# Kernel optimization log

Measured on AMD Instinct MI355X. Metric: run time of the kernel, lower is better.

The kernel has to match this reference:

```python
import jax, jax.numpy as jnp
import numpy as np

B, N, E, D, NS, H = 32, 4096, 256, 256, 8, 256
N_ITERS, N_SH, N_MESH, MESH_LR = 3, 5, 4, 5.0

def layer_norm(x, scale, bias, eps=1e-5):
    m = jnp.mean(x, axis=-1, keepdims=True)
    v = jnp.var(x, axis=-1, keepdims=True)
    return (x - m) / jnp.sqrt(v + eps) * scale + bias

def sinkhorn(C, a, b, u=None, v=None, n_iters=N_SH):
    # log-domain Sinkhorn with marginals a [B,N], b [B,S]; C [B,N,S]
    log_a, log_b = jnp.log(a), jnp.log(b)
    if u is None:
        u = jnp.zeros_like(a)
    if v is None:
        v = jnp.zeros_like(b)
    K = -C
    for _ in range(n_iters):
        u = log_a - jax.nn.logsumexp(K + v[:, None, :], axis=-1)
        v = log_b - jax.nn.logsumexp(K + u[:, :, None], axis=-2)
    attn = jnp.exp(K + u[:, :, None] + v[:, None, :])
    return attn, u, v

def minimize_entropy_of_sinkhorn(C0, a, b, mesh_lr=MESH_LR, n_mesh=N_MESH):
    # MESH: gradient-descend the cost matrix to minimize entropy of the transport plan
    def ent(C):
        attn, _, _ = sinkhorn(C, a, b)
        return -jnp.sum(attn * jnp.log(attn + 1e-8))
    C = C0
    for _ in range(n_mesh):
        C = C - mesh_lr * jax.grad(ent)(C)
    _, u, v = sinkhorn(C, a, b)
    return C, u, v

def gru_cell(x, h, Wih, Whh, bih, bhh):
    # torch.nn.GRUCell math, gate order (r, z, n)
    gi = x @ Wih.T + bih
    gh = h @ Whh.T + bhh
    ir, iz, inn = jnp.split(gi, 3, axis=-1)
    hr, hz, hn = jnp.split(gh, 3, axis=-1)
    r = jax.nn.sigmoid(ir + hr)
    z = jax.nn.sigmoid(iz + hz)
    n = jnp.tanh(inn + r * hn)
    return (1.0 - z) * n + z * h

def setup_inputs():
    key = jax.random.key(0)
    ks = jax.random.split(key, 16)
    s = 0.02
    return {
        "inputs": jax.random.normal(ks[0], (B, N, E), jnp.float32),
        "slots_init": jax.random.normal(ks[1], (B, NS, D), jnp.float32),
        "ln_in_s": jnp.ones((E,), jnp.float32), "ln_in_b": jnp.zeros((E,), jnp.float32),
        "ln_sl_s": jnp.ones((D,), jnp.float32), "ln_sl_b": jnp.zeros((D,), jnp.float32),
        "ln_mlp_s": jnp.ones((D,), jnp.float32), "ln_mlp_b": jnp.zeros((D,), jnp.float32),
        "Wq": jax.random.normal(ks[2], (D, D), jnp.float32) * s,
        "Wk": jax.random.normal(ks[3], (E, D), jnp.float32) * s,
        "Wv": jax.random.normal(ks[4], (E, D), jnp.float32) * s,
        "wi_W": jax.random.normal(ks[5], (E, 1), jnp.float32) * s, "wi_b": jnp.zeros((1,), jnp.float32),
        "ws_W": jax.random.normal(ks[6], (D, 1), jnp.float32) * s, "ws_b": jnp.zeros((1,), jnp.float32),
        "gru_Wih": jax.random.normal(ks[7], (3 * D, D), jnp.float32) * s,
        "gru_Whh": jax.random.normal(ks[8], (3 * D, D), jnp.float32) * s,
        "gru_bih": jnp.zeros((3 * D,), jnp.float32), "gru_bhh": jnp.zeros((3 * D,), jnp.float32),
        "mlp_W1": jax.random.normal(ks[9], (D, H), jnp.float32) * s, "mlp_b1": jnp.zeros((H,), jnp.float32),
        "mlp_W2": jax.random.normal(ks[10], (H, D), jnp.float32) * s, "mlp_b2": jnp.zeros((D,), jnp.float32),
    }

def reference(inputs, slots_init, ln_in_s, ln_in_b, ln_sl_s, ln_sl_b, ln_mlp_s, ln_mlp_b, Wq, Wk, Wv, wi_W, wi_b, ws_W, ws_b, gru_Wih, gru_Whh, gru_bih, gru_bhh, mlp_W1, mlp_b1, mlp_W2, mlp_b2):
    x = layer_norm(inputs, ln_in_s, ln_in_b)
    k = x @ Wk          # [B,N,D]
    v = x @ Wv          # [B,N,D]
    a = jax.nn.softmax(jnp.squeeze(x @ wi_W, -1) + wi_b[0], axis=-1) * NS  # input marginal [B,N]
    k_sq = jnp.sum(k * k, axis=-1)  # [B,N]

    def step(slots):
        sn = layer_norm(slots, ln_sl_s, ln_sl_b)
        b = jax.nn.softmax(jnp.squeeze(sn @ ws_W, -1) + ws_b[0], axis=-1) * NS  # slot marginal [B,S]
        q = sn @ Wq  # [B,S,D]
        # Euclidean cdist(k, q) via the Gram-matrix identity
        d2 = k_sq[:, :, None] + jnp.sum(q * q, -1)[:, None, :] - 2.0 * jnp.einsum('bnd,bsd->bns', k, q)
        C = jnp.sqrt(jnp.clip(d2, 1e-12))
        C, p, qpot = minimize_entropy_of_sinkhorn(C, a, b)
        attn, _, _ = sinkhorn(C, a, b, u=p, v=qpot)  # warm-started final sinkhorn
        updates = jnp.einsum('bns,bnd->bsd', attn, v)
        h = gru_cell(updates.reshape(-1, D), slots.reshape(-1, D), gru_Wih, gru_Whh, gru_bih, gru_bhh).reshape(B, NS, D)
        hn = layer_norm(h, ln_mlp_s, ln_mlp_b)
        h = h + (jax.nn.relu(hn @ mlp_W1 + mlp_b1) @ mlp_W2 + mlp_b2)
        return h, attn

    slots = slots_init
    attn = None
    for _ in range(N_ITERS - 1):
        slots, attn = step(slots)
    slots = jax.lax.stop_gradient(slots)  # .detach() before final step
    slots, attn = step(slots)
    return slots, jnp.transpose(attn, (0, 2, 1)), slots
```

## Files before the change

kernel.cpp:

```cpp
#include <hip/hip_runtime.h>
#include <hip/hip_bf16.h>

#define B_ 32
#define N_ 4096
#define E_ 256
#define D_ 256
#define NS_ 8
#define LN8 2.0794415416798357f
#define OFF_ATTN 65536
#define OFF_S2   (65536 + 1048576)
#define NSPLIT 8
#define SENT 0xFFFFFFFFu

typedef unsigned short u16;
typedef unsigned short u16x8 __attribute__((ext_vector_type(8)));
typedef __bf16 bf16x8 __attribute__((ext_vector_type(8)));
typedef float floatx4 __attribute__((ext_vector_type(4)));

__device__ __forceinline__ float bf2f(u16 h) {
  unsigned int u = ((unsigned int)h) << 16;
  return __uint_as_float(u);
}
__device__ __forceinline__ u16 f2bf(float f) {
  unsigned int u = __float_as_uint(f);
  unsigned int r = (u + 0x7FFFu + ((u >> 16) & 1u)) >> 16;
  return (u16)r;
}
__device__ __forceinline__ float ldx(const void* p, int i, int dt) {
  return dt ? ((const float*)p)[i] : bf2f(((const u16*)p)[i]);
}
__device__ __forceinline__ void stx(void* p, size_t i, int dt, float v) {
  if (dt) ((float*)p)[i] = v; else ((u16*)p)[i] = f2bf(v);
}
__device__ __forceinline__ float slog(float x) { return __logf(fmaxf(x, 1e-35f)); }
__device__ __forceinline__ float cl(float x) { return fminf(fmaxf(x, -1e30f), 1e30f); }

__device__ __forceinline__ float breduce256(float v, float* red4, int tid) {
  #pragma unroll
  for (int m = 1; m < 64; m <<= 1) v += __shfl_xor(v, m, 64);
  __syncthreads();
  if ((tid & 63) == 0) red4[tid >> 6] = v;
  __syncthreads();
  return red4[0] + red4[1] + red4[2] + red4[3];
}

__device__ __forceinline__ float breduce768(float v, float* red4, int tid) {
  #pragma unroll
  for (int m = 1; m < 64; m <<= 1) v += __shfl_xor(v, m, 64);
  __syncthreads();
  if (tid < 256 && (tid & 63) == 0) red4[tid >> 6] = v;
  __syncthreads();
  return red4[0] + red4[1] + red4[2] + red4[3];
}

__global__ void detect_dtype_kernel(const u16* __restrict__ inp, int* __restrict__ flag) {
  int lane = threadIdx.x & 63;
  int good = 0;
  for (int i = lane; i < 256; i += 64) {
    float x = bf2f(inp[i]);
    float ax = fabsf(x);
    if (x == 0.0f || (ax >= 1e-3f && ax <= 64.0f)) good++;
  }
  #pragma unroll
  for (int m = 1; m < 64; m <<= 1) good += __shfl_xor(good, m, 64);
  if (lane == 0) *flag = (good >= 208) ? 0 : 1;
}


__global__ void tr_kv_kernel(const void* __restrict__ Wk, const void* __restrict__ Wv,
                             u16* __restrict__ WkvT, const int* __restrict__ dtf) {
  const int dt = *dtf;
  int idx = blockIdx.x * 256 + threadIdx.x;
  int half = idx >> 16, i = idx & 65535;
  int r = i >> 8, c = i & 255;
  const void* src = half ? Wv : Wk;
  WkvT[((size_t)(half * 256 + c)) * 256 + r] = f2bf(ldx(src, i, dt));
}

__global__ void cast_w_kernel(const void* __restrict__ Wih, const void* __restrict__ Whh,
                              u16* __restrict__ WihB, u16* __restrict__ WhhB,
                              const int* __restrict__ dtf) {
  const int dt = *dtf;
  int idx = blockIdx.x * 256 + threadIdx.x;
  int half = idx >= 196608;
  int i = idx - (half ? 196608 : 0);
  u16* dst = half ? WhhB : WihB;
  dst[i] = f2bf(ldx(half ? Whh : Wih, i, dt));
}

__global__ void cast_slots_kernel(const void* __restrict__ src, float* __restrict__ dst,
                                  const int* __restrict__ dtf) {
  const int dt = *dtf;
  int i = blockIdx.x * 256 + threadIdx.x;
  dst[i] = ldx(src, i, dt);
}

__global__ __launch_bounds__(256) void ln_stats_kernel(
    const void* __restrict__ inp, const void* __restrict__ lns, const void* __restrict__ lnb,
    const void* __restrict__ wiW, const int* __restrict__ dtf,
    u16* __restrict__ xln, float* __restrict__ logits) {
  const int dt = *dtf;
  int row = blockIdx.x * 4 + (threadIdx.x >> 6);
  int lane = threadIdx.x & 63;
  float xs[4];
  if (dt) {
    float4 h = *(const float4*)((const float*)inp + (size_t)row * E_ + lane * 4);
    xs[0] = h.x; xs[1] = h.y; xs[2] = h.z; xs[3] = h.w;
  } else {
    ushort4 h = *(const ushort4*)((const u16*)inp + (size_t)row * E_ + lane * 4);
    xs[0] = bf2f(h.x); xs[1] = bf2f(h.y); xs[2] = bf2f(h.z); xs[3] = bf2f(h.w);
  }
  float s = xs[0] + xs[1] + xs[2] + xs[3];
  float q = xs[0]*xs[0] + xs[1]*xs[1] + xs[2]*xs[2] + xs[3]*xs[3];
  #pragma unroll
  for (int m = 1; m < 64; m <<= 1) { s += __shfl_xor(s, m, 64); q += __shfl_xor(q, m, 64); }
  float mean = s * (1.0f / E_);
  float var = q * (1.0f / E_) - mean * mean;
  float rstd = rsqrtf(fmaxf(var, 0.0f) + 1e-5f);
  int e = lane * 4;
  float d = 0.0f;
  float xn[4];
  #pragma unroll
  for (int j = 0; j < 4; ++j) {
    xn[j] = (xs[j] - mean) * rstd * ldx(lns, e + j, dt) + ldx(lnb, e + j, dt);
    d += xn[j] * ldx(wiW, e + j, dt);
  }
  ushort4 o;
  o.x = f2bf(xn[0]); o.y = f2bf(xn[1]); o.z = f2bf(xn[2]); o.w = f2bf(xn[3]);
  *(ushort4*)(xln + (size_t)row * E_ + e) = o;
  #pragma unroll
  for (int m = 1; m < 64; m <<= 1) d += __shfl_xor(d, m, 64);
  if (lane == 0) logits[row] = d;
}

__global__ __launch_bounds__(1024) void amarg_kernel(const float* __restrict__ logits,
    float* __restrict__ log_a, float* __restrict__ inva) {
  __shared__ float red[16];
  __shared__ float bcast;
  int b = blockIdx.x, tid = threadIdx.x;
  logits += (size_t)b * N_;
  float l[4];
  #pragma unroll
  for (int i = 0; i < 4; ++i) l[i] = logits[tid + i * 1024];
  float mx = fmaxf(fmaxf(l[0], l[1]), fmaxf(l[2], l[3]));
  #pragma unroll
  for (int m = 1; m < 64; m <<= 1) mx = fmaxf(mx, __shfl_xor(mx, m, 64));
  __syncthreads();
  if ((tid & 63) == 0) red[tid >> 6] = mx;
  __syncthreads();
  if (tid == 0) { float v = red[0]; for (int i = 1; i < 16; ++i) v = fmaxf(v, red[i]); bcast = v; }
  __syncthreads();
  float M = bcast;
  float se = 0.0f;
  #pragma unroll
  for (int i = 0; i < 4; ++i) se += __expf(l[i] - M);
  #pragma unroll
  for (int m = 1; m < 64; m <<= 1) se += __shfl_xor(se, m, 64);
  __syncthreads();
  if ((tid & 63) == 0) red[tid >> 6] = se;
  __syncthreads();
  if (tid == 0) { float v = 0; for (int i = 0; i < 16; ++i) v += red[i]; bcast = v; }
  __syncthreads();
  float lgS = slog(bcast);
  #pragma unroll
  for (int i = 0; i < 4; ++i) {
    float lav = l[i] - M - lgS + LN8;
    log_a[tid + i * 1024] = lav;
    inva[tid + i * 1024] = fminf(__expf(-lav), 1e20f);
  }
}

__global__ __launch_bounds__(256, 2) void gemm_bt_kernel(
    const u16* __restrict__ A, const u16* __restrict__ BT,
    u16* __restrict__ kbf, u16* __restrict__ vbf) {
  __shared__ __align__(16) u16 Als[128 * 32];
  __shared__ __align__(16) u16 Bls[128 * 32];
  int tid = threadIdx.x;
  int m0 = blockIdx.x * 128, n0 = blockIdx.y * 128;
  u16* ob = (n0 < 256) ? kbf : vbf;
  int nb = n0 & 255;
  int w = tid >> 6, lane = tid & 63;
  int wm = (w & 1) * 64, wn = (w >> 1) * 64;
  int fr = lane & 15, kg = lane >> 4;
  floatx4 acc[4][4];
  #pragma unroll
  for (int i = 0; i < 4; ++i)
    #pragma unroll
    for (int j = 0; j < 4; ++j) acc[i][j] = (floatx4){0.f, 0.f, 0.f, 0.f};
  int sm = tid >> 1;
  int sk0 = (tid & 1) * 16;
  const u16* arow = A + (size_t)(m0 + sm) * E_;
  const u16* brow = BT + (size_t)(n0 + sm) * E_;
  for (int kc = 0; kc < E_; kc += 32) {
    #pragma unroll
    for (int j = 0; j < 16; j += 8) {
      int kk = kc + sk0 + j;
      *(u16x8*)&Als[sm * 32 + sk0 + j] = *(const u16x8*)(arow + kk);
      *(u16x8*)&Bls[sm * 32 + sk0 + j] = *(const u16x8*)(brow + kk);
    }
    __syncthreads();
    bf16x8 af[4], bfv[4];
    #pragma unroll
    for (int im = 0; im < 4; ++im) af[im] = *(const bf16x8*)&Als[(wm + im * 16 + fr) * 32 + kg * 8];
    #pragma unroll
    for (int in = 0; in < 4; ++in) bfv[in] = *(const bf16x8*)&Bls[(wn + in * 16 + fr) * 32 + kg * 8];
    #pragma unroll
    for (int im = 0; im < 4; ++im)
      #pragma unroll
      for (int in = 0; in < 4; ++in)
        acc[im][in] = __builtin_amdgcn_mfma_f32_16x16x32_bf16(af[im], bfv[in], acc[im][in], 0, 0, 0);
    __syncthreads();
  }
  #pragma unroll
  for (int im = 0; im < 4; ++im)
    #pragma unroll
    for (int in = 0; in < 4; ++in)
      #pragma unroll
      for (int r = 0; r < 4; ++r) {
        int row = m0 + wm + im * 16 + kg * 4 + r;
        int col = nb + wn + in * 16 + fr;
        ob[(size_t)row * D_ + col] = f2bf(acc[im][in][r]);
      }
}


__global__ __launch_bounds__(256) void s1_kernel(
    const float* __restrict__ slots, const void* __restrict__ lnss, const void* __restrict__ lnsb,
    const void* __restrict__ Wq, const void* __restrict__ wsW, const int* __restrict__ dtf,
    float* __restrict__ qf, float* __restrict__ q_sq, float* __restrict__ logits_b) {
  __shared__ float sn_sh[256];
  __shared__ float red4[4];
  const int dt = *dtf;
  int row = blockIdx.x;
  int tid = threadIdx.x;
  float h = slots[(size_t)row * D_ + tid];
  float sum = breduce256(h, red4, tid);
  float sq = breduce256(h * h, red4, tid);
  float mean = sum * (1.0f / D_), var = sq * (1.0f / D_) - mean * mean;
  float rstd = rsqrtf(fmaxf(var, 0.0f) + 1e-5f);
  float sn = (h - mean) * rstd * ldx(lnss, tid, dt) + ldx(lnsb, tid, dt);
  sn_sh[tid] = sn;
  __syncthreads();
  float acc = 0.0f;
  if (dt) {
    const float* W = (const float*)Wq;
    for (int d = 0; d < 256; ++d) acc += sn_sh[d] * W[d * 256 + tid];
  } else {
    const u16* W = (const u16*)Wq;
    for (int d = 0; d < 256; ++d) acc += sn_sh[d] * bf2f(W[d * 256 + tid]);
  }
  qf[(size_t)row * 256 + tid] = acc;
  float qs = breduce256(acc * acc, red4, tid);
  float lbp = breduce256(sn * ldx(wsW, tid, dt), red4, tid);
  if (tid == 0) { q_sq[row] = qs; logits_b[row] = lbp; }
}

__device__ __forceinline__ float grp_sync_reduce(
    float acc8[8], float (*red)[8],
    unsigned int* gp, int rp, int blkn, int wv, int lane, int tid) {
  #pragma unroll
  for (int m = 1; m < 64; m <<= 1)
    #pragma unroll
    for (int s = 0; s < 8; ++s) acc8[s] += __shfl_xor(acc8[s], m, 64);
  if (lane == 0)
    #pragma unroll
    for (int s = 0; s < 8; ++s) red[wv][s] = acc8[s];
  __syncthreads();
  float x = 0.0f;
  if (tid < 64) {
    float v = red[tid >> 3][tid & 7];
    v += __shfl_xor(v, 8, 64);
    v += __shfl_xor(v, 16, 64);
    v += __shfl_xor(v, 32, 64);
    if (tid < 8)
      __hip_atomic_store(gp + rp * 64 + blkn * 8 + tid, __float_as_uint(v),
                         __ATOMIC_RELAXED, __HIP_MEMORY_SCOPE_AGENT);
    unsigned int u;
    for (;;) {
      u = __hip_atomic_load(gp + rp * 64 + tid, __ATOMIC_RELAXED, __HIP_MEMORY_SCOPE_AGENT);
      if (__all(u != SENT)) break;
      __builtin_amdgcn_s_sleep(1);
    }
    x = __uint_as_float(u);
    x += __shfl_xor(x, 8, 64);
    x += __shfl_xor(x, 16, 64);
    x += __shfl_xor(x, 32, 64);
  }
  return x;
}

__global__ __launch_bounds__(512, 2) void mesh_kernel(
    const u16* __restrict__ kbf, const u16* __restrict__ vbf,
    const float* __restrict__ qf32, const float* __restrict__ qsq_g,
    const float* __restrict__ log_a_g, const float* __restrict__ inva_g,
    const float* __restrict__ logits_b_g, const void* __restrict__ wsb,
    const int* __restrict__ dtf,
    unsigned int* __restrict__ gpart,
    float* __restrict__ updp, void* __restrict__ dout_or_null) {
  const int blkn = blockIdx.x;
  const int b = blockIdx.y;
  const int tid = threadIdx.x;
  const int dt = *dtf;
  const int n = blkn * 512 + tid;

  __shared__ float evP[6][8];
  __shared__ float lb[8], invb[8];
  __shared__ float dv[8];
  __shared__ float red[8][8];
  __shared__ float q_lds[8][256];
  __shared__ float qsq_l[8];
  __shared__ float pv_lds[512][8];

  const float la = log_a_g[(size_t)b * N_ + n];
  const float ia = inva_g[(size_t)b * N_ + n];
  unsigned int* gp = gpart + (size_t)b * 64 * 64;

  {
    const float* qb = qf32 + (size_t)b * 8 * 256;
    #pragma unroll
    for (int i = tid; i < 2048; i += 512) q_lds[i >> 8][i & 255] = qb[i];
    if (tid < 8) {
      qsq_l[tid] = qsq_g[b * 8 + tid];
      float off = ldx(wsb, 0, dt);
      float l[8], M = -1e30f;
      #pragma unroll
      for (int s = 0; s < 8; ++s) { l[s] = logits_b_g[b * 8 + s] + off; M = fmaxf(M, l[s]); }
      float S = 0.0f;
      #pragma unroll
      for (int s = 0; s < 8; ++s) S += __expf(l[s] - M);
      float lgS = slog(S);
      float x = l[tid] - M - lgS + LN8;
      lb[tid] = x; invb[tid] = fminf(__expf(-x), 1e20f);
    }
  }
  __syncthreads();

  float E[8], dK[8], eus[5];
  float eu = 0.0f, dup = 0.0f;
  {
    const u16* kp = kbf + ((size_t)b * N_ + n) * D_;
    float accq[8] = {0, 0, 0, 0, 0, 0, 0, 0};
    float kq = 0.0f;
    for (int kc = 0; kc < 256; kc += 8) {
      u16x8 kv = *(const u16x8*)(kp + kc);
      float kf[8];
      #pragma unroll
      for (int j = 0; j < 8; ++j) { kf[j] = bf2f(kv[j]); kq += kf[j] * kf[j]; }
      #pragma unroll
      for (int s = 0; s < 8; ++s) {
        float4 qa = *(const float4*)&q_lds[s][kc];
        float4 qb2 = *(const float4*)&q_lds[s][kc + 4];
        accq[s] += kf[0] * qa.x + kf[1] * qa.y + kf[2] * qa.z + kf[3] * qa.w
                 + kf[4] * qb2.x + kf[5] * qb2.y + kf[6] * qb2.z + kf[7] * qb2.w;
      }
    }
    #pragma unroll
    for (int s = 0; s < 8; ++s) {
      float d2 = kq + qsq_l[s] - 2.0f * accq[s];
      float Cv = sqrtf(fmaxf(d2, 1e-12f));
      E[s] = __expf(-Cv);
    }
  }

  const int wv = tid >> 6, lane = tid & 63;
  int rp = 0;

  for (int mesh = 0; mesh < 4; ++mesh) {
    if (tid < 8) evP[0][tid] = 1.0f;
    __syncthreads();
    for (int t = 1; t <= 5; ++t) {
      float evp[8];
      #pragma unroll
      for (int s = 0; s < 8; ++s) evp[s] = evP[t - 1][s];
      float su = 0.0f;
      #pragma unroll
      for (int s = 0; s < 8; ++s) su += fminf(E[s] * evp[s], 1e30f);
      float u = la - slog(su);
      eu = fminf(__expf(u), 1e20f);
      eus[t - 1] = eu;
      float acc8[8];
      #pragma unroll
      for (int s = 0; s < 8; ++s) acc8[s] = fminf(E[s] * eu, 1e30f);
      float S = grp_sync_reduce(acc8, red, gp, rp, blkn, wv, lane, tid);
      if (tid < 8) {
        float v = lb[tid] - slog(S);
        evP[t][tid] = fminf(__expf(v), 1e20f);
      }
      ++rp;
      __syncthreads();
    }
    {
      float ev5[8];
      #pragma unroll
      for (int s = 0; s < 8; ++s) ev5[s] = evP[5][s];
      float acc8[8];
      dup = 0.0f;
      #pragma unroll
      for (int s = 0; s < 8; ++s) {
        float t1 = fminf(E[s] * eu, 1e30f);
        float P = fminf(t1 * ev5[s], 1e30f);
        float Pe = P + 1e-8f;
        float g = -(__logf(Pe) + P / Pe) * P;
        dK[s] = g; dup += g; acc8[s] = g;
      }
      float S = grp_sync_reduce(acc8, red, gp, rp, blkn, wv, lane, tid);
      if (tid < 8) dv[tid] = cl(S);
      ++rp;
      __syncthreads();
    }
    for (int t = 5; t >= 1; --t) {
      float evt[8], evtm[8], dvl[8], ibl[8];
      #pragma unroll
      for (int s = 0; s < 8; ++s) { evt[s] = evP[t][s]; evtm[s] = evP[t - 1][s]; dvl[s] = dv[s]; ibl[s] = invb[s]; }
      float eut = eus[t - 1];
      float duv = 0.0f;
      float w8[8];
      #pragma unroll
      for (int s = 0; s < 8; ++s) {
        float a1 = fminf(E[s] * eut, 1e30f);
        float b1 = fminf(a1 * evt[s], 1e30f);
        w8[s] = fminf(b1 * ibl[s], 1e30f);
        duv += cl(dvl[s] * w8[s]);
      }
      float du = ((t == 5) ? dup : 0.0f) - duv;
      float duf = cl(cl(du * ia) * eut);
      float acc8[8];
      #pragma unroll
      for (int s = 0; s < 8; ++s) {
        float ee = fminf(E[s] * evtm[s], 1e30f);
        float zc = cl(ee * duf);
        dK[s] -= cl(dvl[s] * w8[s]) + zc;
        acc8[s] = -zc;
      }
      if (t > 1) {
        float S = grp_sync_reduce(acc8, red, gp, rp, blkn, wv, lane, tid);
        if (tid < 8) dv[tid] = cl(S);
        ++rp;
      }
      __syncthreads();
    }
    #pragma unroll
    for (int s = 0; s < 8; ++s) {
      float dkc = fminf(fmaxf(dK[s], -4.0f), 4.0f);
      float Enew = E[s] * __expf(-5.0f * dkc);
      E[s] = fminf(fmaxf(Enew, 1e-35f), 1e30f);
    }
  }

  if (tid < 8) evP[0][tid] = 1.0f;
  __syncthreads();
  for (int t = 1; t <= 10; ++t) {
    int pc = (t - 1) & 1, cc = t & 1;
    float evp[8];
    #pragma unroll
    for (int s = 0; s < 8; ++s) evp[s] = evP[pc][s];
    float su = 0.0f;
    #pragma unroll
    for (int s = 0; s < 8; ++s) su += fminf(E[s] * evp[s], 1e30f);
    eu = fminf(__expf(la - slog(su)), 1e20f);
    float acc8[8];
    #pragma unroll
    for (int s = 0; s < 8; ++s) acc8[s] = fminf(E[s] * eu, 1e30f);
    float S = grp_sync_reduce(acc8, red, gp, rp, blkn, wv, lane, tid);
    if (tid < 8) {
      float v = lb[tid] - slog(S);
      evP[cc][tid] = fminf(__expf(v), 1e20f);
    }
    ++rp;
    __syncthreads();
  }
  float evf[8];
  #pragma unroll
  for (int s = 0; s < 8; ++s) evf[s] = evP[0][s];
  float pv[8];
  #pragma unroll
  for (int s = 0; s < 8; ++s) {
    float t1 = fminf(E[s] * eu, 1e30f);
    pv[s] = fminf(t1 * evf[s], 1e30f);
  }
  if (dout_or_null) {
    #pragma unroll
    for (int s = 0; s < 8; ++s)
      stx(dout_or_null, (size_t)OFF_ATTN + ((size_t)b * 8 + s) * N_ + n, dt, pv[s]);
  }

  #pragma unroll
  for (int s = 0; s < 8; ++s) pv_lds[tid][s] = pv[s];
  __syncthreads();
  {
    int d = tid & 255, half = tid >> 8;
    const u16* vp = vbf + ((size_t)b * N_ + blkn * 512 + half * 256) * D_ + d;
    float acc[8] = {0, 0, 0, 0, 0, 0, 0, 0};
    for (int i = 0; i < 256; ++i) {
      float vv = bf2f(vp[(size_t)i * D_]);
      float4 a0 = *(const float4*)&pv_lds[half * 256 + i][0];
      float4 a1 = *(const float4*)&pv_lds[half * 256 + i][4];
      acc[0] += a0.x * vv; acc[1] += a0.y * vv; acc[2] += a0.z * vv; acc[3] += a0.w * vv;
      acc[4] += a1.x * vv; acc[5] += a1.y * vv; acc[6] += a1.z * vv; acc[7] += a1.w * vv;
    }
    __syncthreads();
    if (half == 1) {
      #pragma unroll
      for (int s = 0; s < 8; ++s) pv_lds[d][s] = acc[s];
    }
    __syncthreads();
    if (half == 0) {
      #pragma unroll
      for (int s = 0; s < 8; ++s) acc[s] += pv_lds[d][s];
      #pragma unroll
      for (int s = 0; s < 8; ++s)
        updp[(((size_t)b * 8 + blkn) * 8 + s) * D_ + d] = acc[s];
    }
  }
}

__global__ __launch_bounds__(768) void gru_s1_kernel(
    const float* __restrict__ updp, const float* __restrict__ slots_cur,
    const u16* __restrict__ WihB, const u16* __restrict__ WhhB,
    const void* __restrict__ bih, const void* __restrict__ bhh,
    const void* __restrict__ lnms, const void* __restrict__ lnmb,
    const void* __restrict__ W1, const void* __restrict__ b1,
    const void* __restrict__ W2, const void* __restrict__ b2,
    const void* __restrict__ lnss, const void* __restrict__ lnsb,
    const void* __restrict__ Wq, const void* __restrict__ wsW,
    const int* __restrict__ dtf, int do_s1,
    float* __restrict__ slots_next, float* __restrict__ qf,
    float* __restrict__ q_sq, float* __restrict__ logits_b,
    void* __restrict__ dout_or_null) {
  __shared__ float xs[256], hs[256], hns[256], as_[256];
  __shared__ float gi_sh[768], gh_sh[768];
  __shared__ float red4[4];
  const int dt = *dtf;
  int row = blockIdx.x;
  int b = row >> 3, s = row & 7;
  int tid = threadIdx.x;
  if (tid < 256) {
    float x = 0.0f;
    #pragma unroll
    for (int c = 0; c < 8; ++c) x += updp[(((size_t)b * 8 + c) * 8 + s) * D_ + tid];
    xs[tid] = x;
    hs[tid] = slots_cur[(size_t)row * D_ + tid];
  }
  __syncthreads();
  {
    float gi = ldx(bih, tid, dt);
    float gh = ldx(bhh, tid, dt);
    const u16* wi = WihB + (size_t)tid * 256;
    const u16* wh = WhhB + (size_t)tid * 256;
    for (int e = 0; e < 256; e += 8) {
      u16x8 a = *(const u16x8*)(wi + e);
      u16x8 c = *(const u16x8*)(wh + e);
      #pragma unroll
      for (int j = 0; j < 8; ++j) gi += xs[e + j] * bf2f(a[j]);
      #pragma unroll
      for (int j = 0; j < 8; ++j) gh += hs[e + j] * bf2f(c[j]);
    }
    gi_sh[tid] = gi; gh_sh[tid] = gh;
  }
  __syncthreads();
  float h2 = 0.0f;
  if (tid < 256) {
    float r = 1.0f / (1.0f + __expf(-(gi_sh[tid] + gh_sh[tid])));
    float z = 1.0f / (1.0f + __expf(-(gi_sh[256 + tid] + gh_sh[256 + tid])));
    float nn = tanhf(gi_sh[512 + tid] + r * gh_sh[512 + tid]);
    h2 = (1.0f - z) * nn + z * hs[tid];
  }
  float sum = breduce768(h2, red4, tid);
  float sq = breduce768(h2 * h2, red4, tid);
  float mean = sum * (1.0f / D_), var = sq * (1.0f / D_) - mean * mean;
  float rstd = rsqrtf(fmaxf(var, 0.0f) + 1e-5f);
  if (tid < 256) {
    float hn2 = (h2 - mean) * rstd * ldx(lnms, tid, dt) + ldx(lnmb, tid, dt);
    hns[tid] = hn2;
  }
  __syncthreads();
  float o = 0.0f;
  if (tid < 256) {
    float a1 = ldx(b1, tid, dt);
    if (dt) {
      const float* W = (const float*)W1;
      for (int e = 0; e < 256; ++e) a1 += hns[e] * W[e * 256 + tid];
    } else {
      const u16* W = (const u16*)W1;
      for (int e = 0; e < 256; ++e) a1 += hns[e] * bf2f(W[e * 256 + tid]);
    }
    as_[tid] = fmaxf(a1, 0.0f);
  }
  __syncthreads();
  if (tid < 256) {
    o = h2 + ldx(b2, tid, dt);
    if (dt) {
      const float* W = (const float*)W2;
      for (int e = 0; e < 256; ++e) o += as_[e] * W[e * 256 + tid];
    } else {
      const u16* W = (const u16*)W2;
      for (int e = 0; e < 256; ++e) o += as_[e] * bf2f(W[e * 256 + tid]);
    }
    slots_next[(size_t)row * D_ + tid] = o;
    if (dout_or_null) {
      stx(dout_or_null, (size_t)row * D_ + tid, dt, o);
      stx(dout_or_null, (size_t)OFF_S2 + (size_t)row * D_ + tid, dt, o);
    }
  }
  if (do_s1) {
    float sum2 = breduce768(o, red4, tid);
    float sq2 = breduce768(o * o, red4, tid);
    float mean2 = sum2 * (1.0f / D_), var2 = sq2 * (1.0f / D_) - mean2 * mean2;
    float rstd2 = rsqrtf(fmaxf(var2, 0.0f) + 1e-5f);
    float sn = 0.0f;
    __syncthreads();
    if (tid < 256) {
      sn = (o - mean2) * rstd2 * ldx(lnss, tid, dt) + ldx(lnsb, tid, dt);
      xs[tid] = sn;
    }
    __syncthreads();
    float accq = 0.0f;
    if (tid < 256) {
      if (dt) {
        const float* W = (const float*)Wq;
        for (int d = 0; d < 256; ++d) accq += xs[d] * W[d * 256 + tid];
      } else {
        const u16* W = (const u16*)Wq;
        for (int d = 0; d < 256; ++d) accq += xs[d] * bf2f(W[d * 256 + tid]);
      }
      qf[(size_t)row * 256 + tid] = accq;
    }
    float qs = breduce768(accq * accq, red4, tid);
    float lbp = breduce768(tid < 256 ? sn * ldx(wsW, tid, dt) : 0.0f, red4, tid);
    if (tid == 0) { q_sq[row] = qs; logits_b[row] = lbp; }
  }
}


extern "C" void kernel_launch(void* const* d_in, const int* in_sizes, int n_in,
                              void* d_out, int out_size, void* d_ws, size_t ws_size,
                              hipStream_t stream) {
  (void)in_sizes; (void)n_in; (void)out_size;
  const void* inp      = d_in[0];
  const void* slots0   = d_in[1];
  const void* ln_in_s  = d_in[2];
  const void* ln_in_b  = d_in[3];
  const void* ln_sl_s  = d_in[4];
  const void* ln_sl_b  = d_in[5];
  const void* ln_mlp_s = d_in[6];
  const void* ln_mlp_b = d_in[7];
  const void* Wq  = d_in[8];
  const void* Wk  = d_in[9];
  const void* Wv  = d_in[10];
  const void* wiW = d_in[11];
  const void* wsW = d_in[13];
  const void* wsb = d_in[14];
  const void* Wih = d_in[15];
  const void* Whh = d_in[16];
  const void* bih = d_in[17];
  const void* bhh = d_in[18];
  const void* W1  = d_in[19];
  const void* b1  = d_in[20];
  const void* W2  = d_in[21];
  const void* b2  = d_in[22];

  char* ws = (char*)d_ws;
  size_t off = 0;
  auto alloc = [&](size_t bytes) -> void* {
    void* p = ws + off;
    off += (bytes + 255) & ~(size_t)255;
    return p;
  };
  const size_t NR = (size_t)B_ * N_;
  int* dtflag     = (int*)alloc(256);
  float* logits_a = (float*)alloc(NR * 4);
  float* log_a    = (float*)alloc(NR * 4);
  float* inva     = (float*)alloc(NR * 4);
  u16* xln        = (u16*)alloc(NR * E_ * 2);
  u16* kbf        = (u16*)alloc(NR * D_ * 2);
  u16* vbf        = (u16*)alloc(NR * D_ * 2);
  u16* WkvT       = (u16*)alloc((size_t)512 * 256 * 2);
  u16* WihB       = (u16*)alloc(768 * 256 * 2);
  u16* WhhB       = (u16*)alloc(768 * 256 * 2);
  float* qf32     = (float*)alloc((size_t)B_ * 8 * 256 * 4);
  float* q_sq     = (float*)alloc(B_ * 8 * 4);
  float* logits_b = (float*)alloc(B_ * 8 * 4);
  float* updp     = (float*)alloc((size_t)B_ * 8 * 8 * D_ * 4);
  float* slots_a  = (float*)alloc((size_t)B_ * 8 * D_ * 4);
  float* slots_b  = (float*)alloc((size_t)B_ * 8 * D_ * 4);
  unsigned int* gpart = (unsigned int*)alloc((size_t)3 * B_ * 64 * 64 * 4);
  if (ws_size < off) return;

  hipMemsetAsync(gpart, 0xFF, (size_t)3 * B_ * 64 * 64 * 4, stream);
  detect_dtype_kernel<<<1, 64, 0, stream>>>((const u16*)inp, dtflag);

  tr_kv_kernel<<<512, 256, 0, stream>>>(Wk, Wv, WkvT, dtflag);
  cast_w_kernel<<<1536, 256, 0, stream>>>(Wih, Whh, WihB, WhhB, dtflag);
  cast_slots_kernel<<<(B_ * 8 * D_) / 256, 256, 0, stream>>>(slots0, slots_a, dtflag);
  ln_stats_kernel<<<NR / 4, 256, 0, stream>>>(inp, ln_in_s, ln_in_b, wiW, dtflag, xln, logits_a);
  amarg_kernel<<<B_, 1024, 0, stream>>>(logits_a, log_a, inva);
  gemm_bt_kernel<<<dim3(NR / 128, 4), 256, 0, stream>>>(xln, WkvT, kbf, vbf);

  float* scur = slots_a;
  float* snext = slots_b;
  s1_kernel<<<B_ * 8, 256, 0, stream>>>(scur, ln_sl_s, ln_sl_b, Wq, wsW, dtflag, qf32, q_sq, logits_b);
  for (int step = 0; step < 3; ++step) {
    bool last = (step == 2);
    mesh_kernel<<<dim3(NSPLIT, B_), 512, 0, stream>>>(kbf, vbf, qf32, q_sq, log_a, inva,
                                                      logits_b, wsb, dtflag,
                                                      gpart + (size_t)step * B_ * 64 * 64,
                                                      updp, last ? d_out : (void*)nullptr);
    gru_s1_kernel<<<B_ * 8, 768, 0, stream>>>(updp, scur, WihB, WhhB, bih, bhh,
                                              ln_mlp_s, ln_mlp_b, W1, b1, W2, b2,
                                              ln_sl_s, ln_sl_b, Wq, wsW, dtflag, last ? 0 : 1,
                                              snext, qf32, q_sq, logits_b,
                                              last ? d_out : (void*)nullptr);
    float* t = scur; scur = snext; snext = t;
  }
}
```

Baseline: 993.2 us.

## Split mesh kernel into head, single-block sinkhorn, and update kernels

New measurement: 1.360 ms. 1.37x slower.

```diff
diff --git a/kernel.cpp b/kernel.cpp
--- a/kernel.cpp
+++ b/kernel.cpp
@@ -10,7 +10,6 @@
 #define OFF_ATTN 65536
 #define OFF_S2   (65536 + 1048576)
 #define NSPLIT 8
-#define SENT 0xFFFFFFFFu
 
 typedef unsigned short u16;
 typedef unsigned short u16x8 __attribute__((ext_vector_type(8)));
@@ -255,72 +254,82 @@
   if (tid == 0) { q_sq[row] = qs; logits_b[row] = lbp; }
 }
 
-__device__ __forceinline__ float grp_sync_reduce(
-    float acc8[8], float (*red)[8],
-    unsigned int* gp, int rp, int blkn, int wv, int lane, int tid) {
-  #pragma unroll
-  for (int m = 1; m < 64; m <<= 1)
-    #pragma unroll
-    for (int s = 0; s < 8; ++s) acc8[s] += __shfl_xor(acc8[s], m, 64);
-  if (lane == 0)
-    #pragma unroll
-    for (int s = 0; s < 8; ++s) red[wv][s] = acc8[s];
-  __syncthreads();
-  float x = 0.0f;
-  if (tid < 64) {
-    float v = red[tid >> 3][tid & 7];
-    v += __shfl_xor(v, 8, 64);
-    v += __shfl_xor(v, 16, 64);
-    v += __shfl_xor(v, 32, 64);
-    if (tid < 8)
-      __hip_atomic_store(gp + rp * 64 + blkn * 8 + tid, __float_as_uint(v),
-                         __ATOMIC_RELAXED, __HIP_MEMORY_SCOPE_AGENT);
-    unsigned int u;
-    for (;;) {
-      u = __hip_atomic_load(gp + rp * 64 + tid, __ATOMIC_RELAXED, __HIP_MEMORY_SCOPE_AGENT);
-      if (__all(u != SENT)) break;
-      __builtin_amdgcn_s_sleep(1);
-    }
-    x = __uint_as_float(u);
-    x += __shfl_xor(x, 8, 64);
-    x += __shfl_xor(x, 16, 64);
-    x += __shfl_xor(x, 32, 64);
-  }
-  return x;
-}
-
-__global__ __launch_bounds__(512, 2) void mesh_kernel(
-    const u16* __restrict__ kbf, const u16* __restrict__ vbf,
-    const float* __restrict__ qf32, const float* __restrict__ qsq_g,
-    const float* __restrict__ log_a_g, const float* __restrict__ inva_g,
-    const float* __restrict__ logits_b_g, const void* __restrict__ wsb,
-    const int* __restrict__ dtf,
-    unsigned int* __restrict__ gpart,
-    float* __restrict__ updp, void* __restrict__ dout_or_null) {
+__global__ __launch_bounds__(512) void head_kernel(
+    const u16* __restrict__ kbf, const float* __restrict__ qf32,
+    const float* __restrict__ qsq_g, float* __restrict__ Ebuf) {
   const int blkn = blockIdx.x;
   const int b = blockIdx.y;
   const int tid = threadIdx.x;
+  const int n = blkn * 512 + tid;
+  __shared__ float q_lds[8][256];
+  __shared__ float qsq_l[8];
+  {
+    const float* qb = qf32 + (size_t)b * 8 * 256;
+    #pragma unroll
+    for (int i = tid; i < 2048; i += 512) q_lds[i >> 8][i & 255] = qb[i];
+    if (tid < 8) qsq_l[tid] = qsq_g[b * 8 + tid];
+  }
+  __syncthreads();
+  const u16* kp = kbf + ((size_t)b * N_ + n) * D_;
+  float accq[8] = {0, 0, 0, 0, 0, 0, 0, 0};
+  float kq = 0.0f;
+  for (int kc = 0; kc < 256; kc += 8) {
+    u16x8 kv = *(const u16x8*)(kp + kc);
+    float kf[8];
+    #pragma unroll
+    for (int j = 0; j < 8; ++j) { kf[j] = bf2f(kv[j]); kq += kf[j] * kf[j]; }
+    #pragma unroll
+    for (int s = 0; s < 8; ++s) {
+      float4 qa = *(const float4*)&q_lds[s][kc];
+      float4 qb2 = *(const float4*)&q_lds[s][kc + 4];
+      accq[s] += kf[0] * qa.x + kf[1] * qa.y + kf[2] * qa.z + kf[3] * qa.w
+               + kf[4] * qb2.x + kf[5] * qb2.y + kf[6] * qb2.z + kf[7] * qb2.w;
+    }
+  }
+  float E[8];
+  #pragma unroll
+  for (int s = 0; s < 8; ++s) {
+    float d2 = kq + qsq_l[s] - 2.0f * accq[s];
+    float Cv = sqrtf(fmaxf(d2, 1e-12f));
+    E[s] = __expf(-Cv);
+  }
+  float* ep = Ebuf + ((size_t)b * N_ + n) * 8;
+  *(float4*)ep = make_float4(E[0], E[1], E[2], E[3]);
+  *(float4*)(ep + 4) = make_float4(E[4], E[5], E[6], E[7]);
+}
+
+__global__ __launch_bounds__(512, 2) void sink_kernel(
+    const float* __restrict__ Ebuf, const float* __restrict__ log_a_g,
+    const float* __restrict__ inva_g, const float* __restrict__ logits_b_g,
+    const void* __restrict__ wsb, const int* __restrict__ dtf,
+    float* __restrict__ attn, void* __restrict__ dout_or_null) {
+  const int b = blockIdx.x;
+  const int tid = threadIdx.x;
   const int dt = *dtf;
-  const int n = blkn * 512 + tid;
+  const int wv = tid >> 6, lane = tid & 63;
 
   __shared__ float evP[6][8];
   __shared__ float lb[8], invb[8];
   __shared__ float dv[8];
   __shared__ float red[8][8];
-  __shared__ float q_lds[8][256];
-  __shared__ float qsq_l[8];
-  __shared__ float pv_lds[512][8];
-
-  const float la = log_a_g[(size_t)b * N_ + n];
-  const float ia = inva_g[(size_t)b * N_ + n];
-  unsigned int* gp = gpart + (size_t)b * 64 * 64;
+  __shared__ float eus_l[5][512][9];
+
+  float E[8][8], dK[8][8];
+  float eu[8], dup[8], la[8], ia[8];
 
   {
-    const float* qb = qf32 + (size_t)b * 8 * 256;
-    #pragma unroll
-    for (int i = tid; i < 2048; i += 512) q_lds[i >> 8][i & 255] = qb[i];
+    const float* ep = Ebuf + (size_t)b * N_ * 8;
+    #pragma unroll
+    for (int r = 0; r < 8; ++r) {
+      int n = r * 512 + tid;
+      float4 c0 = *(const float4*)(ep + (size_t)n * 8);
+      float4 c1 = *(const float4*)(ep + (size_t)n * 8 + 4);
+      E[r][0] = c0.x; E[r][1] = c0.y; E[r][2] = c0.z; E[r][3] = c0.w;
+      E[r][4] = c1.x; E[r][5] = c1.y; E[r][6] = c1.z; E[r][7] = c1.w;
+      la[r] = log_a_g[(size_t)b * N_ + n];
+      ia[r] = inva_g[(size_t)b * N_ + n];
+    }
     if (tid < 8) {
-      qsq_l[tid] = qsq_g[b * 8 + tid];
       float off = ldx(wsb, 0, dt);
       float l[8], M = -1e30f;
       #pragma unroll
@@ -335,35 +344,25 @@
   }
   __syncthreads();
 
-  float E[8], dK[8], eus[5];
-  float eu = 0.0f, dup = 0.0f;
-  {
-    const u16* kp = kbf + ((size_t)b * N_ + n) * D_;
-    float accq[8] = {0, 0, 0, 0, 0, 0, 0, 0};
-    float kq = 0.0f;
-    for (int kc = 0; kc < 256; kc += 8) {
-      u16x8 kv = *(const u16x8*)(kp + kc);
-      float kf[8];
-      #pragma unroll
-      for (int j = 0; j < 8; ++j) { kf[j] = bf2f(kv[j]); kq += kf[j] * kf[j]; }
-      #pragma unroll
-      for (int s = 0; s < 8; ++s) {
-        float4 qa = *(const float4*)&q_lds[s][kc];
-        float4 qb2 = *(const float4*)&q_lds[s][kc + 4];
-        accq[s] += kf[0] * qa.x + kf[1] * qa.y + kf[2] * qa.z + kf[3] * qa.w
-                 + kf[4] * qb2.x + kf[5] * qb2.y + kf[6] * qb2.z + kf[7] * qb2.w;
-      }
-    }
-    #pragma unroll
-    for (int s = 0; s < 8; ++s) {
-      float d2 = kq + qsq_l[s] - 2.0f * accq[s];
-      float Cv = sqrtf(fmaxf(d2, 1e-12f));
-      E[s] = __expf(-Cv);
-    }
-  }
-
-  const int wv = tid >> 6, lane = tid & 63;
-  int rp = 0;
+  auto rsum = [&](float acc8[8]) -> float {
+    #pragma unroll
+    for (int m = 1; m < 64; m <<= 1)
+      #pragma unroll
+      for (int s = 0; s < 8; ++s) acc8[s] += __shfl_xor(acc8[s], m, 64);
+    if (lane == 0)
+      #pragma unroll
+      for (int s = 0; s < 8; ++s) red[wv][s] = acc8[s];
+    __syncthreads();
+    float x = 0.0f;
+    if (tid < 64) {
+      float v = red[tid >> 3][tid & 7];
+      v += __shfl_xor(v, 8, 64);
+      v += __shfl_xor(v, 16, 64);
+      v += __shfl_xor(v, 32, 64);
+      x = v;
+    }
+    return x;
+  };
 
   for (int mesh = 0; mesh < 4; ++mesh) {
     if (tid < 8) evP[0][tid] = 1.0f;
@@ -372,79 +371,89 @@
       float evp[8];
       #pragma unroll
       for (int s = 0; s < 8; ++s) evp[s] = evP[t - 1][s];
-      float su = 0.0f;
-      #pragma unroll
-      for (int s = 0; s < 8; ++s) su += fminf(E[s] * evp[s], 1e30f);
-      float u = la - slog(su);
-      eu = fminf(__expf(u), 1e20f);
-      eus[t - 1] = eu;
-      float acc8[8];
-      #pragma unroll
-      for (int s = 0; s < 8; ++s) acc8[s] = fminf(E[s] * eu, 1e30f);
-      float S = grp_sync_reduce(acc8, red, gp, rp, blkn, wv, lane, tid);
+      float acc8[8] = {0, 0, 0, 0, 0, 0, 0, 0};
+      #pragma unroll
+      for (int r = 0; r < 8; ++r) {
+        float su = 0.0f;
+        #pragma unroll
+        for (int s = 0; s < 8; ++s) su += fminf(E[r][s] * evp[s], 1e30f);
+        float u = la[r] - slog(su);
+        float e_u = fminf(__expf(u), 1e20f);
+        eu[r] = e_u;
+        eus_l[t - 1][tid][r] = e_u;
+        #pragma unroll
+        for (int s = 0; s < 8; ++s) acc8[s] += fminf(E[r][s] * e_u, 1e30f);
+      }
+      float S = rsum(acc8);
       if (tid < 8) {
         float v = lb[tid] - slog(S);
         evP[t][tid] = fminf(__expf(v), 1e20f);
       }
-      ++rp;
       __syncthreads();
     }
     {
       float ev5[8];
       #pragma unroll
       for (int s = 0; s < 8; ++s) ev5[s] = evP[5][s];
-      float acc8[8];
-      dup = 0.0f;
-      #pragma unroll
-      for (int s = 0; s < 8; ++s) {
-        float t1 = fminf(E[s] * eu, 1e30f);
-        float P = fminf(t1 * ev5[s], 1e30f);
-        float Pe = P + 1e-8f;
-        float g = -(__logf(Pe) + P / Pe) * P;
-        dK[s] = g; dup += g; acc8[s] = g;
+      float acc8[8] = {0, 0, 0, 0, 0, 0, 0, 0};
+      #pragma unroll
+      for (int r = 0; r < 8; ++r) {
+        float ds = 0.0f;
+        #pragma unroll
+        for (int s = 0; s < 8; ++s) {
+          float t1 = fminf(E[r][s] * eu[r], 1e30f);
+          float P = fminf(t1 * ev5[s], 1e30f);
+          float Pe = P + 1e-8f;
+          float g = -(__logf(Pe) + P / Pe) * P;
+          dK[r][s] = g; ds += g; acc8[s] += g;
+        }
+        dup[r] = ds;
       }
-      float S = grp_sync_reduce(acc8, red, gp, rp, blkn, wv, lane, tid);
+      float S = rsum(acc8);
       if (tid < 8) dv[tid] = cl(S);
-      ++rp;
       __syncthreads();
     }
     for (int t = 5; t >= 1; --t) {
       float evt[8], evtm[8], dvl[8], ibl[8];
       #pragma unroll
       for (int s = 0; s < 8; ++s) { evt[s] = evP[t][s]; evtm[s] = evP[t - 1][s]; dvl[s] = dv[s]; ibl[s] = invb[s]; }
-      float eut = eus[t - 1];
-      float duv = 0.0f;
-      float w8[8];
-      #pragma unroll
-      for (int s = 0; s < 8; ++s) {
-        float a1 = fminf(E[s] * eut, 1e30f);
-        float b1 = fminf(a1 * evt[s], 1e30f);
-        w8[s] = fminf(b1 * ibl[s], 1e30f);
-        duv += cl(dvl[s] * w8[s]);
-      }
-      float du = ((t == 5) ? dup : 0.0f) - duv;
-      float duf = cl(cl(du * ia) * eut);
-      float acc8[8];
-      #pragma unroll
-      for (int s = 0; s < 8; ++s) {
-        float ee = fminf(E[s] * evtm[s], 1e30f);
-        float zc = cl(ee * duf);
-        dK[s] -= cl(dvl[s] * w8[s]) + zc;
-        acc8[s] = -zc;
+      float acc8[8] = {0, 0, 0, 0, 0, 0, 0, 0};
+      #pragma unroll
+      for (int r = 0; r < 8; ++r) {
+        float eut = eus_l[t - 1][tid][r];
+        float duv = 0.0f;
+        float w8[8];
+        #pragma unroll
+        for (int s = 0; s < 8; ++s) {
+          float a1 = fminf(E[r][s] * eut, 1e30f);
+          float b1 = fminf(a1 * evt[s], 1e30f);
+          w8[s] = fminf(b1 * ibl[s], 1e30f);
+          duv += cl(dvl[s] * w8[s]);
+        }
+        float du = ((t == 5) ? dup[r] : 0.0f) - duv;
+        float duf = cl(cl(du * ia[r]) * eut);
+        #pragma unroll
+        for (int s = 0; s < 8; ++s) {
+          float ee = fminf(E[r][s] * evtm[s], 1e30f);
+          float zc = cl(ee * duf);
+          dK[r][s] -= cl(dvl[s] * w8[s]) + zc;
+          acc8[s] -= zc;
+        }
       }
       if (t > 1) {
-        float S = grp_sync_reduce(acc8, red, gp, rp, blkn, wv, lane, tid);
+        float S = rsum(acc8);
         if (tid < 8) dv[tid] = cl(S);
-        ++rp;
       }
       __syncthreads();
     }
     #pragma unroll
-    for (int s = 0; s < 8; ++s) {
-      float dkc = fminf(fmaxf(dK[s], -4.0f), 4.0f);
-      float Enew = E[s] * __expf(-5.0f * dkc);
-      E[s] = fminf(fmaxf(Enew, 1e-35f), 1e30f);
-    }
+    for (int r = 0; r < 8; ++r)
+      #pragma unroll
+      for (int s = 0; s < 8; ++s) {
+        float dkc = fminf(fmaxf(dK[r][s], -4.0f), 4.0f);
+        float Enew = E[r][s] * __expf(-5.0f * dkc);
+        E[r][s] = fminf(fmaxf(Enew, 1e-35f), 1e30f);
+      }
   }
 
   if (tid < 8) evP[0][tid] = 1.0f;
@@ -454,64 +463,62 @@
     float evp[8];
     #pragma unroll
     for (int s = 0; s < 8; ++s) evp[s] = evP[pc][s];
-    float su = 0.0f;
-    #pragma unroll
-    for (int s = 0; s < 8; ++s) su += fminf(E[s] * evp[s], 1e30f);
-    eu = fminf(__expf(la - slog(su)), 1e20f);
-    float acc8[8];
-    #pragma unroll
-    for (int s = 0; s < 8; ++s) acc8[s] = fminf(E[s] * eu, 1e30f);
-    float S = grp_sync_reduce(acc8, red, gp, rp, blkn, wv, lane, tid);
+    float acc8[8] = {0, 0, 0, 0, 0, 0, 0, 0};
+    #pragma unroll
+    for (int r = 0; r < 8; ++r) {
+      float su = 0.0f;
+      #pragma unroll
+      for (int s = 0; s < 8; ++s) su += fminf(E[r][s] * evp[s], 1e30f);
+      eu[r] = fminf(__expf(la[r] - slog(su)), 1e20f);
+      #pragma unroll
+      for (int s = 0; s < 8; ++s) acc8[s] += fminf(E[r][s] * eu[r], 1e30f);
+    }
+    float S = rsum(acc8);
     if (tid < 8) {
       float v = lb[tid] - slog(S);
       evP[cc][tid] = fminf(__expf(v), 1e20f);
     }
-    ++rp;
     __syncthreads();
   }
   float evf[8];
   #pragma unroll
   for (int s = 0; s < 8; ++s) evf[s] = evP[0][s];
-  float pv[8];
-  #pragma unroll
-  for (int s = 0; s < 8; ++s) {
-    float t1 = fminf(E[s] * eu, 1e30f);
-    pv[s] = fminf(t1 * evf[s], 1e30f);
-  }
-  if (dout_or_null) {
-    #pragma unroll
-    for (int s = 0; s < 8; ++s)
-      stx(dout_or_null, (size_t)OFF_ATTN + ((size_t)b * 8 + s) * N_ + n, dt, pv[s]);
-  }
-
-  #pragma unroll
-  for (int s = 0; s < 8; ++s) pv_lds[tid][s] = pv[s];
-  __syncthreads();
-  {
-    int d = tid & 255, half = tid >> 8;
-    const u16* vp = vbf + ((size_t)b * N_ + blkn * 512 + half * 256) * D_ + d;
-    float acc[8] = {0, 0, 0, 0, 0, 0, 0, 0};
-    for (int i = 0; i < 256; ++i) {
-      float vv = bf2f(vp[(size_t)i * D_]);
-      float4 a0 = *(const float4*)&pv_lds[half * 256 + i][0];
-      float4 a1 = *(const float4*)&pv_lds[half * 256 + i][4];
-      acc[0] += a0.x * vv; acc[1] += a0.y * vv; acc[2] += a0.z * vv; acc[3] += a0.w * vv;
-      acc[4] += a1.x * vv; acc[5] += a1.y * vv; acc[6] += a1.z * vv; acc[7] += a1.w * vv;
-    }
-    __syncthreads();
-    if (half == 1) {
-      #pragma unroll
-      for (int s = 0; s < 8; ++s) pv_lds[d][s] = acc[s];
-    }
-    __syncthreads();
-    if (half == 0) {
-      #pragma unroll
-      for (int s = 0; s < 8; ++s) acc[s] += pv_lds[d][s];
+  #pragma unroll
+  for (int r = 0; r < 8; ++r) {
+    int n = r * 512 + tid;
+    float pv[8];
+    #pragma unroll
+    for (int s = 0; s < 8; ++s) {
+      float t1 = fminf(E[r][s] * eu[r], 1e30f);
+      pv[s] = fminf(t1 * evf[s], 1e30f);
+    }
+    float* ap = attn + ((size_t)b * N_ + n) * 8;
+    *(float4*)ap = make_float4(pv[0], pv[1], pv[2], pv[3]);
+    *(float4*)(ap + 4) = make_float4(pv[4], pv[5], pv[6], pv[7]);
+    if (dout_or_null) {
       #pragma unroll
       for (int s = 0; s < 8; ++s)
-        updp[(((size_t)b * 8 + blkn) * 8 + s) * D_ + d] = acc[s];
-    }
-  }
+        stx(dout_or_null, (size_t)OFF_ATTN + ((size_t)b * 8 + s) * N_ + n, dt, pv[s]);
+    }
+  }
+}
+
+__global__ __launch_bounds__(256) void upd_kernel(
+    const float* __restrict__ attn, const u16* __restrict__ vbf, float* __restrict__ updp) {
+  int chunk = blockIdx.x, b = blockIdx.y, d = threadIdx.x;
+  const float* ap = attn + ((size_t)b * N_ + chunk * 512) * 8;
+  const u16* vp = vbf + ((size_t)b * N_ + chunk * 512) * D_ + d;
+  float acc[8] = {0, 0, 0, 0, 0, 0, 0, 0};
+  for (int i = 0; i < 512; ++i) {
+    float4 a0 = *(const float4*)(ap + (size_t)i * 8);
+    float4 a1 = *(const float4*)(ap + (size_t)i * 8 + 4);
+    float vv = bf2f(vp[(size_t)i * D_]);
+    acc[0] += a0.x * vv; acc[1] += a0.y * vv; acc[2] += a0.z * vv; acc[3] += a0.w * vv;
+    acc[4] += a1.x * vv; acc[5] += a1.y * vv; acc[6] += a1.z * vv; acc[7] += a1.w * vv;
+  }
+  #pragma unroll
+  for (int s = 0; s < 8; ++s)
+    updp[(((size_t)b * 8 + chunk) * 8 + s) * D_ + d] = acc[s];
 }
 
 __global__ __launch_bounds__(768) void gru_s1_kernel(
@@ -680,13 +687,13 @@
   float* qf32     = (float*)alloc((size_t)B_ * 8 * 256 * 4);
   float* q_sq     = (float*)alloc(B_ * 8 * 4);
   float* logits_b = (float*)alloc(B_ * 8 * 4);
+  float* Ebuf     = (float*)alloc(NR * 8 * 4);
+  float* attnb    = (float*)alloc(NR * 8 * 4);
   float* updp     = (float*)alloc((size_t)B_ * 8 * 8 * D_ * 4);
   float* slots_a  = (float*)alloc((size_t)B_ * 8 * D_ * 4);
   float* slots_b  = (float*)alloc((size_t)B_ * 8 * D_ * 4);
-  unsigned int* gpart = (unsigned int*)alloc((size_t)3 * B_ * 64 * 64 * 4);
   if (ws_size < off) return;
 
-  hipMemsetAsync(gpart, 0xFF, (size_t)3 * B_ * 64 * 64 * 4, stream);
   detect_dtype_kernel<<<1, 64, 0, stream>>>((const u16*)inp, dtflag);
 
   tr_kv_kernel<<<512, 256, 0, stream>>>(Wk, Wv, WkvT, dtflag);
@@ -701,10 +708,10 @@
   s1_kernel<<<B_ * 8, 256, 0, stream>>>(scur, ln_sl_s, ln_sl_b, Wq, wsW, dtflag, qf32, q_sq, logits_b);
   for (int step = 0; step < 3; ++step) {
     bool last = (step == 2);
-    mesh_kernel<<<dim3(NSPLIT, B_), 512, 0, stream>>>(kbf, vbf, qf32, q_sq, log_a, inva,
-                                                      logits_b, wsb, dtflag,
-                                                      gpart + (size_t)step * B_ * 64 * 64,
-                                                      updp, last ? d_out : (void*)nullptr);
+    head_kernel<<<dim3(NSPLIT, B_), 512, 0, stream>>>(kbf, qf32, q_sq, Ebuf);
+    sink_kernel<<<B_, 512, 0, stream>>>(Ebuf, log_a, inva, logits_b, wsb, dtflag,
+                                        attnb, last ? d_out : (void*)nullptr);
+    upd_kernel<<<dim3(8, B_), 256, 0, stream>>>(attnb, vbf, updp);
     gru_s1_kernel<<<B_ * 8, 768, 0, stream>>>(updp, scur, WihB, WhhB, bih, bhh,
                                               ln_mlp_s, ln_mlp_b, W1, b1, W2, b2,
                                               ln_sl_s, ln_sl_b, Wq, wsW, dtflag, last ? 0 : 1,
```
